# Optimization experiments

Hardware: AMD Instinct MI355X
Metric: run time of the kernel (lower is better)

The kernel has to match this reference:

```python
import jax, jax.numpy as jnp
import numpy as np

RADIUS = 0.2
NSAMPLE = 32


def ball_query(radius, nsample, xyz, new_xyz):
    # xyz: (B, N, 3), new_xyz: (B, M, 3) -> idx: (B, M, nsample) int32
    N = xyz.shape[1]
    # squared distances (B, M, N)
    d2 = jnp.sum((new_xyz[:, :, None, :] - xyz[:, None, :, :]) ** 2, axis=-1)
    # key = point index if within radius else N (sentinel); take nsample smallest keys
    key = jnp.where(d2 < radius * radius, jnp.arange(N, dtype=jnp.int32), N)
    neg_top, _ = jax.lax.top_k(-key, nsample)  # ascending keys = earliest in-radius indices
    idx = -neg_top  # (B, M, nsample)
    valid = idx < N
    first = idx[..., :1]
    first = jnp.where(first < N, first, 0)  # if ball empty, fall back to index 0
    return jnp.where(valid, idx, first)


def group_points(features, idx):
    # features: (B, C, N), idx: (B, M, S) -> (B, C, M, S)
    return jax.vmap(lambda f, i: f[:, i])(features, idx)


def setup_inputs() -> dict:
    key = jax.random.key(0)
    k1, k2, k3 = jax.random.split(key, 3)
    B, N, M, C = 4, 16384, 2048, 64
    xyz = jax.random.uniform(k1, (B, N, 3), dtype=jnp.float32)
    new_xyz = jax.random.uniform(k2, (B, M, 3), dtype=jnp.float32)
    features = jax.random.normal(k3, (B, C, N), dtype=jnp.float32)
    return {"xyz": xyz, "new_xyz": new_xyz, "features": features}


def reference(xyz, new_xyz, features):
    idx = ball_query(RADIUS, NSAMPLE, xyz, new_xyz)  # (B, M, S)
    xyz_t = jnp.transpose(xyz, (0, 2, 1))  # (B, 3, N)
    grouped_xyz = group_points(xyz_t, idx)  # (B, 3, M, S)
    grouped_xyz = grouped_xyz - jnp.transpose(new_xyz, (0, 2, 1))[..., None]
    grouped_features = group_points(features, idx)  # (B, C, M, S)
    # use_xyz=True: concat relative coordinates with grouped features
    return jnp.concatenate([grouped_xyz, grouped_features], axis=1)  # (B, 3+C, M, S)
```

## Files before the change

### kernel.cpp

```cpp
#include <hip/hip_runtime.h>


typedef float vf4 __attribute__((ext_vector_type(4)));

#define WPB 2
constexpr int Bc = 4, Nc = 16384, Mc = 2048, Cc = 64, Sc = 32;
constexpr int NQ = Bc * Mc;

__global__ __launch_bounds__(256) void prep_kernel(
    const float* __restrict__ feat,
    const float* __restrict__ xyz,
    float* __restrict__ featT,
    vf4* __restrict__ xyz4)
{
    if (blockIdx.y == Bc) {
        const int t = blockIdx.x * 256 + threadIdx.x;
        const float* p = xyz + (size_t)t * 3;
        vf4 v; v.x = p[0]; v.y = p[1]; v.z = p[2]; v.w = 0.0f;
        xyz4[t] = v;
        return;
    }
    __shared__ float tile[64][65];
    const int b = blockIdx.y;
    const int nbase = blockIdx.x * 64;
    const int tn = threadIdx.x & 63;
    const int tq = threadIdx.x >> 6;
    const float* fb = feat + (size_t)b * Cc * Nc;
    float* ob = featT + (size_t)b * Nc * Cc;
    #pragma unroll
    for (int k = 0; k < 16; ++k) {
        const int c = k * 4 + tq;
        tile[tn][c] = fb[(size_t)c * Nc + nbase + tn];
    }
    __syncthreads();
    #pragma unroll
    for (int k = 0; k < 16; ++k) {
        const int nl = k * 4 + tq;
        ob[(size_t)(nbase + nl) * Cc + tn] = tile[nl][tn];
    }
}

__global__ __launch_bounds__(128) void qg_kernel(
    const vf4* __restrict__ xyz4,
    const float* __restrict__ new_xyz,
    const float* __restrict__ featT,
    float* __restrict__ out)
{
#pragma clang fp contract(off)
    const int lane = threadIdx.x & 63;
    const int wv   = threadIdx.x >> 6;

    const int xcd = blockIdx.x & 7;
    const int b   = xcd >> 1;
    const int m   = ((xcd & 1) << 10) + (blockIdx.x >> 3) * WPB + wv;

    __shared__ int sidx[WPB][Sc];

    const float r2 = 0.2f * 0.2f;
    const float* nz = new_xyz + (size_t)(b * Mc + m) * 3;
    const float qx = nz[0], qy = nz[1], qz = nz[2];
    const vf4* xb4 = xyz4 + (size_t)b * Nc;

    int count = 0, firstIdx = 0;
    const unsigned long long lt = (1ull << lane) - 1ull;

    vf4 pv[4];
    #pragma unroll
    for (int u = 0; u < 4; ++u) pv[u] = xb4[u * 64 + lane];
    for (int base = 0; base < Nc; base += 256) {
        const int nb = (base + 256 < Nc) ? base + 256 : base;
        vf4 nv[4];
        #pragma unroll
        for (int u = 0; u < 4; ++u) nv[u] = xb4[nb + u * 64 + lane];
        #pragma unroll
        for (int u = 0; u < 4; ++u) {
            const float dx = qx - pv[u].x, dy = qy - pv[u].y, dz = qz - pv[u].z;
            float d2 = dx * dx + dy * dy;
            d2 = d2 + dz * dz;
            const bool in = d2 < r2;
            const unsigned long long mask = __ballot(in);
            if (in) {
                const int slot = count + __popcll(mask & lt);
                if (slot < Sc) sidx[wv][slot] = base + u * 64 + lane;
            }
            if (count == 0 && mask != 0ull)
                firstIdx = base + u * 64 + __builtin_ctzll(mask);
            count += __popcll(mask);
        }
        if (count >= Sc) break;
        #pragma unroll
        for (int u = 0; u < 4; ++u) pv[u] = nv[u];
    }
    {
        const int start = count < Sc ? count : Sc;
        if (start + lane < Sc) sidx[wv][start + lane] = firstIdx;
    }
    asm volatile("s_waitcnt lgkmcnt(0)" ::: "memory");

    const int s     = lane & 31;
    const int chalf = lane >> 5;
    const int myid  = sidx[wv][s];
    float* ob = out + ((size_t)b * 67 * Mc + m) * Sc;

    const float* ftb = featT + ((size_t)b * Nc + myid) * Cc;
    vf4 vr[8];
    #pragma unroll
    for (int it = 0; it < 8; ++it)
        vr[it] = *(const vf4*)(ftb + (it * 2 + chalf) * 4);
    const vf4 p = xb4[myid];

    if (chalf == 0) {
        __builtin_nontemporal_store(p.x - qx, &ob[(size_t)0 * (Mc * Sc) + s]);
        __builtin_nontemporal_store(p.z - qz, &ob[(size_t)2 * (Mc * Sc) + s]);
    } else {
        __builtin_nontemporal_store(p.y - qy, &ob[(size_t)1 * (Mc * Sc) + s]);
    }

    #pragma unroll
    for (int it = 0; it < 8; ++it) {
        const int c4 = it * 2 + chalf;
        #pragma unroll
        for (int k = 0; k < 4; ++k)
            __builtin_nontemporal_store(
                vr[it][k], &ob[(size_t)(3 + c4 * 4 + k) * (Mc * Sc) + s]);
    }
}

__global__ __launch_bounds__(256) void qg_fallback_kernel(
    const float* __restrict__ xyz, const float* __restrict__ new_xyz,
    const float* __restrict__ feat, float* __restrict__ out)
{
#pragma clang fp contract(off)
    const int lane = threadIdx.x & 63;
    const int wv   = threadIdx.x >> 6;
    const int q    = blockIdx.x * 4 + wv;
    const int b    = q >> 11;
    const int m    = q & (Mc - 1);
    __shared__ int sidx[4][Sc];
    const float r2 = 0.2f * 0.2f;
    const float* nz = new_xyz + (size_t)(b * Mc + m) * 3;
    const float qx = nz[0], qy = nz[1], qz = nz[2];
    const float* xb = xyz + (size_t)b * Nc * 3;
    int count = 0, firstIdx = 0;
    const unsigned long long lt = (1ull << lane) - 1ull;
    for (int base = 0; base < Nc; base += 64) {
        const int i = base + lane;
        const float px = xb[i * 3], py = xb[i * 3 + 1], pz = xb[i * 3 + 2];
        const float dx = qx - px, dy = qy - py, dz = qz - pz;
        float d2 = dx * dx + dy * dy; d2 = d2 + dz * dz;
        const bool in = d2 < r2;
        const unsigned long long mask = __ballot(in);
        if (in) {
            const int slot = count + __popcll(mask & lt);
            if (slot < Sc) sidx[wv][slot] = i;
        }
        if (count == 0 && mask != 0ull) firstIdx = base + __builtin_ctzll(mask);
        count += __popcll(mask);
        if (count >= Sc) break;
    }
    const int start = count < Sc ? count : Sc;
    if (start + lane < Sc) sidx[wv][start + lane] = firstIdx;
    asm volatile("s_waitcnt lgkmcnt(0)" ::: "memory");
    const int s = lane & 31, chalf = lane >> 5;
    const int myid = sidx[wv][s];
    float* ob = out + ((size_t)b * 67 * Mc + m) * Sc;
    ob[(size_t)chalf * (Mc * Sc) + s] = xb[(size_t)myid * 3 + chalf] - (chalf ? qy : qx);
    if (chalf == 0)
        ob[(size_t)2 * (Mc * Sc) + s] = xb[(size_t)myid * 3 + 2] - qz;
    const float* fb = feat + (size_t)b * Cc * Nc;
    #pragma unroll
    for (int it = 0; it < 32; ++it) {
        const int c = it * 2 + chalf;
        ob[(size_t)(3 + c) * (Mc * Sc) + s] = fb[(size_t)c * Nc + myid];
    }
}

extern "C" void kernel_launch(void* const* d_in, const int* in_sizes, int n_in,
                              void* d_out, int out_size, void* d_ws, size_t ws_size,
                              hipStream_t stream) {
    const float* xyz     = (const float*)d_in[0];
    const float* new_xyz = (const float*)d_in[1];
    const float* feat    = (const float*)d_in[2];
    float* out           = (float*)d_out;

    const size_t featT_bytes = (size_t)Bc * Nc * Cc * sizeof(float);
    const size_t xyz4_bytes  = (size_t)Bc * Nc * sizeof(vf4);

    if (ws_size >= featT_bytes + xyz4_bytes) {
        float* featT = (float*)d_ws;
        vf4*   xyz4  = (vf4*)((char*)d_ws + featT_bytes);
        hipLaunchKernelGGL(prep_kernel, dim3(Nc / 64, Bc + 1), dim3(256), 0, stream,
                           feat, xyz, featT, xyz4);
        hipLaunchKernelGGL(qg_kernel, dim3(NQ / WPB), dim3(128), 0, stream,
                           xyz4, new_xyz, featT, out);
    } else {
        hipLaunchKernelGGL(qg_fallback_kernel, dim3(NQ / 4), dim3(256), 0, stream,
                           xyz, new_xyz, feat, out);
    }
}
```

Before: 34.66 us.

## Overlap feature transpose with ball-query scan and split out the feature gather

Moves the ball-query scan into the same launch as the feature transpose, so the scan blocks run alongside the transpose blocks. The scan now reads the raw AoS xyz directly instead of a padded float4 copy. It writes the neighbour indices and relative xyz to global memory, and a second kernel gathers the transposed features using those indices. This drops the xyz4 prep pass and hides scan latency behind the transpose. In exchange it adds an index round trip through global memory, uses uncoalesced stride-3 loads in the scan, and gives up the XCD-aware block mapping for the scan.

```diff
diff --git a/kernel.cpp b/kernel.cpp
--- a/kernel.cpp
+++ b/kernel.cpp
@@ -3,78 +3,75 @@
 
 typedef float vf4 __attribute__((ext_vector_type(4)));
 
-#define WPB 2
 constexpr int Bc = 4, Nc = 16384, Mc = 2048, Cc = 64, Sc = 32;
 constexpr int NQ = Bc * Mc;
-
-__global__ __launch_bounds__(256) void prep_kernel(
+constexpr int TB = (Nc / 64) * Bc;
+constexpr int SB = NQ / 4;
+
+__global__ __launch_bounds__(256) void k1_prep_scan(
+    const float* __restrict__ xyz,
+    const float* __restrict__ new_xyz,
     const float* __restrict__ feat,
-    const float* __restrict__ xyz,
     float* __restrict__ featT,
-    vf4* __restrict__ xyz4)
-{
-    if (blockIdx.y == Bc) {
-        const int t = blockIdx.x * 256 + threadIdx.x;
-        const float* p = xyz + (size_t)t * 3;
-        vf4 v; v.x = p[0]; v.y = p[1]; v.z = p[2]; v.w = 0.0f;
-        xyz4[t] = v;
-        return;
-    }
-    __shared__ float tile[64][65];
-    const int b = blockIdx.y;
-    const int nbase = blockIdx.x * 64;
-    const int tn = threadIdx.x & 63;
-    const int tq = threadIdx.x >> 6;
-    const float* fb = feat + (size_t)b * Cc * Nc;
-    float* ob = featT + (size_t)b * Nc * Cc;
-    #pragma unroll
-    for (int k = 0; k < 16; ++k) {
-        const int c = k * 4 + tq;
-        tile[tn][c] = fb[(size_t)c * Nc + nbase + tn];
-    }
-    __syncthreads();
-    #pragma unroll
-    for (int k = 0; k < 16; ++k) {
-        const int nl = k * 4 + tq;
-        ob[(size_t)(nbase + nl) * Cc + tn] = tile[nl][tn];
-    }
-}
-
-__global__ __launch_bounds__(128) void qg_kernel(
-    const vf4* __restrict__ xyz4,
-    const float* __restrict__ new_xyz,
-    const float* __restrict__ featT,
+    int* __restrict__ idxws,
     float* __restrict__ out)
 {
 #pragma clang fp contract(off)
+    __shared__ float tile[64][65];
+    __shared__ int sidx[4][Sc];
+
+    if (blockIdx.x < TB) {
+        const int b = blockIdx.x >> 8;
+        const int nbase = (blockIdx.x & 255) * 64;
+        const int tn = threadIdx.x & 63;
+        const int tq = threadIdx.x >> 6;
+        const float* fb = feat + (size_t)b * Cc * Nc;
+        float* ob = featT + (size_t)b * Nc * Cc;
+        #pragma unroll
+        for (int k = 0; k < 16; ++k) {
+            const int c = k * 4 + tq;
+            tile[tn][c] = fb[(size_t)c * Nc + nbase + tn];
+        }
+        __syncthreads();
+        #pragma unroll
+        for (int k = 0; k < 16; ++k) {
+            const int nl = k * 4 + tq;
+            ob[(size_t)(nbase + nl) * Cc + tn] = tile[nl][tn];
+        }
+        return;
+    }
+
     const int lane = threadIdx.x & 63;
     const int wv   = threadIdx.x >> 6;
-
-    const int xcd = blockIdx.x & 7;
-    const int b   = xcd >> 1;
-    const int m   = ((xcd & 1) << 10) + (blockIdx.x >> 3) * WPB + wv;
-
-    __shared__ int sidx[WPB][Sc];
+    const int q    = (blockIdx.x - TB) * 4 + wv;
+    const int b    = q >> 11;
+    const int m    = q & (Mc - 1);
 
     const float r2 = 0.2f * 0.2f;
     const float* nz = new_xyz + (size_t)(b * Mc + m) * 3;
     const float qx = nz[0], qy = nz[1], qz = nz[2];
-    const vf4* xb4 = xyz4 + (size_t)b * Nc;
+    const float* xb = xyz + (size_t)b * Nc * 3;
 
     int count = 0, firstIdx = 0;
     const unsigned long long lt = (1ull << lane) - 1ull;
 
-    vf4 pv[4];
-    #pragma unroll
-    for (int u = 0; u < 4; ++u) pv[u] = xb4[u * 64 + lane];
+    float px[4], py[4], pz[4];
+    #pragma unroll
+    for (int u = 0; u < 4; ++u) {
+        const float* pp = xb + (size_t)(u * 64 + lane) * 3;
+        px[u] = pp[0]; py[u] = pp[1]; pz[u] = pp[2];
+    }
     for (int base = 0; base < Nc; base += 256) {
         const int nb = (base + 256 < Nc) ? base + 256 : base;
-        vf4 nv[4];
-        #pragma unroll
-        for (int u = 0; u < 4; ++u) nv[u] = xb4[nb + u * 64 + lane];
+        float nx[4], ny[4], nzv[4];
         #pragma unroll
         for (int u = 0; u < 4; ++u) {
-            const float dx = qx - pv[u].x, dy = qy - pv[u].y, dz = qz - pv[u].z;
+            const float* pp = xb + (size_t)(nb + u * 64 + lane) * 3;
+            nx[u] = pp[0]; ny[u] = pp[1]; nzv[u] = pp[2];
+        }
+        #pragma unroll
+        for (int u = 0; u < 4; ++u) {
+            const float dx = qx - px[u], dy = qy - py[u], dz = qz - pz[u];
             float d2 = dx * dx + dy * dy;
             d2 = d2 + dz * dz;
             const bool in = d2 < r2;
@@ -89,33 +86,55 @@
         }
         if (count >= Sc) break;
         #pragma unroll
-        for (int u = 0; u < 4; ++u) pv[u] = nv[u];
+        for (int u = 0; u < 4; ++u) { px[u] = nx[u]; py[u] = ny[u]; pz[u] = nzv[u]; }
     }
     {
         const int start = count < Sc ? count : Sc;
         if (start + lane < Sc) sidx[wv][start + lane] = firstIdx;
     }
     asm volatile("s_waitcnt lgkmcnt(0)" ::: "memory");
+
+    if (lane < Sc) idxws[(size_t)q * Sc + lane] = sidx[wv][lane];
 
     const int s     = lane & 31;
     const int chalf = lane >> 5;
     const int myid  = sidx[wv][s];
     float* ob = out + ((size_t)b * 67 * Mc + m) * Sc;
+    if (chalf == 0) {
+        __builtin_nontemporal_store(xb[(size_t)myid * 3 + 0] - qx,
+                                    &ob[(size_t)0 * (Mc * Sc) + s]);
+        __builtin_nontemporal_store(xb[(size_t)myid * 3 + 2] - qz,
+                                    &ob[(size_t)2 * (Mc * Sc) + s]);
+    } else {
+        __builtin_nontemporal_store(xb[(size_t)myid * 3 + 1] - qy,
+                                    &ob[(size_t)1 * (Mc * Sc) + s]);
+    }
+}
+
+__global__ __launch_bounds__(256) void k2_gather(
+    const float* __restrict__ featT,
+    const int* __restrict__ idxws,
+    float* __restrict__ out)
+{
+    const int lane = threadIdx.x & 63;
+    const int wv   = threadIdx.x >> 6;
+
+    const int xcd = blockIdx.x & 7;
+    const int b   = xcd >> 1;
+    const int m   = ((xcd & 1) << 10) + (blockIdx.x >> 3) * 4 + wv;
+    const int q   = b * Mc + m;
+
+    const int s     = lane & 31;
+    const int chalf = lane >> 5;
+    const int myid  = idxws[(size_t)q * Sc + s];
 
     const float* ftb = featT + ((size_t)b * Nc + myid) * Cc;
     vf4 vr[8];
     #pragma unroll
     for (int it = 0; it < 8; ++it)
         vr[it] = *(const vf4*)(ftb + (it * 2 + chalf) * 4);
-    const vf4 p = xb4[myid];
-
-    if (chalf == 0) {
-        __builtin_nontemporal_store(p.x - qx, &ob[(size_t)0 * (Mc * Sc) + s]);
-        __builtin_nontemporal_store(p.z - qz, &ob[(size_t)2 * (Mc * Sc) + s]);
-    } else {
-        __builtin_nontemporal_store(p.y - qy, &ob[(size_t)1 * (Mc * Sc) + s]);
-    }
-
+
+    float* ob = out + ((size_t)b * 67 * Mc + m) * Sc;
     #pragma unroll
     for (int it = 0; it < 8; ++it) {
         const int c4 = it * 2 + chalf;
@@ -184,15 +203,15 @@
     float* out           = (float*)d_out;
 
     const size_t featT_bytes = (size_t)Bc * Nc * Cc * sizeof(float);
-    const size_t xyz4_bytes  = (size_t)Bc * Nc * sizeof(vf4);
-
-    if (ws_size >= featT_bytes + xyz4_bytes) {
+    const size_t idx_bytes   = (size_t)NQ * Sc * sizeof(int);
+
+    if (ws_size >= featT_bytes + idx_bytes) {
         float* featT = (float*)d_ws;
-        vf4*   xyz4  = (vf4*)((char*)d_ws + featT_bytes);
-        hipLaunchKernelGGL(prep_kernel, dim3(Nc / 64, Bc + 1), dim3(256), 0, stream,
-                           feat, xyz, featT, xyz4);
-        hipLaunchKernelGGL(qg_kernel, dim3(NQ / WPB), dim3(128), 0, stream,
-                           xyz4, new_xyz, featT, out);
+        int*   idxws = (int*)((char*)d_ws + featT_bytes);
+        hipLaunchKernelGGL(k1_prep_scan, dim3(TB + SB), dim3(256), 0, stream,
+                           xyz, new_xyz, feat, featT, idxws, out);
+        hipLaunchKernelGGL(k2_gather, dim3(NQ / 4), dim3(256), 0, stream,
+                           featT, idxws, out);
     } else {
         hipLaunchKernelGGL(qg_fallback_kernel, dim3(NQ / 4), dim3(256), 0, stream,
                            xyz, new_xyz, feat, out);
```

Measured after the change: 38.28 us. 1.1x slower.
